# Optimization experiments

Measured on AMD Instinct MI355X. Metric: run time of the kernel, lower is better.

The kernel has to match this reference:

```python
import jax, jax.numpy as jnp
import numpy as np

P = 16384        # nodes per detector layer
NLAYERS = 5      # conf.nlayers (layer labels 0..NLAYERS)
NPROP = 1        # conf.model.nprop
D, S, H = 64, 16, 256   # dyn_features, static_features, deeplayer_nodes
E = 262144       # edges per edge-set (avg degree 16)
NG = 64          # num_graphs


def setup_inputs() -> dict:
    key = jax.random.key(0)
    ks = jax.random.split(key, 20)
    N = P * (NLAYERS + 1)
    F = D + S
    sc = 0.05
    ri = lambda k, shape: jax.random.randint(k, shape, 0, P, dtype=jnp.int32)
    return {
        "x0": jax.random.normal(ks[0], (N, 1), jnp.float32),
        "static": jax.random.normal(ks[1], (N, S), jnp.float32),
        "W1": jax.random.normal(ks[2], (4, F, H), jnp.float32) * sc,
        "b1": jax.random.normal(ks[3], (4, H), jnp.float32) * sc,
        "W2": jax.random.normal(ks[4], (4, H, H), jnp.float32) * sc,
        "b2": jax.random.normal(ks[5], (4, H), jnp.float32) * sc,
        "W3": jax.random.normal(ks[6], (4, H, D), jnp.float32) * sc,
        "b3": jax.random.normal(ks[7], (4, D), jnp.float32) * sc,
        "eps": jnp.zeros((3,), jnp.float32),
        "lin_w": jax.random.normal(ks[8], (D, 1), jnp.float32) * sc,
        "lin_b": jax.random.normal(ks[9], (1,), jnp.float32) * sc,
        "inner_src": ri(ks[10], (NLAYERS, E)),
        "inner_dst": ri(ks[11], (NLAYERS, E)),
        "fwd_src": ri(ks[12], (NLAYERS - 1, E)),
        "fwd_dst": ri(ks[13], (NLAYERS - 1, E)),
        "bwd_src": ri(ks[14], (NLAYERS - 1, E)),
        "bwd_dst": ri(ks[15], (NLAYERS - 1, E)),
        "batch_idx": jax.random.randint(ks[16], (N,), 0, NG, dtype=jnp.int32),
        "num_graphs": NG,
    }


def reference(x0, static, W1, b1, W2, b2, W3, b3, eps, lin_w, lin_b,
              inner_src, inner_dst, fwd_src, fwd_dst, bwd_src, bwd_dst,
              batch_idx, num_graphs):
    N = x0.shape[0]

    def mlp(i, h):
        # dnn(): Linear(F,H)+ReLU, Linear(H,H)+ReLU, Linear(H,D)+ReLU
        h = jax.nn.relu(h @ W1[i] + b1[i])
        h = jax.nn.relu(h @ W2[i] + b2[i])
        return jax.nn.relu(h @ W3[i] + b3[i])

    def gin(i, xs, src, dst):
        # GINConv(train_eps=True): mlp((1+eps)*x + sum_{j in N(v)} x_j)
        aggr = jax.ops.segment_sum(xs[src], dst, num_segments=xs.shape[0])
        return mlp(i, (1.0 + eps[i]) * xs + aggr)

    # x = hstack(batch.x, zeros(N, D-1))
    x = jnp.concatenate([x0, jnp.zeros((N, D - 1), x0.dtype)], axis=1)

    for _ in range(NPROP):
        for il in range(NLAYERS):
            s0 = il * P
            # inner conv on layer il (addstatic over that layer's nodes)
            xs = jnp.concatenate([x[s0:s0 + P], static[s0:s0 + P]], axis=1)
            x = x.at[s0:s0 + P].set(gin(0, xs, inner_src[il], inner_dst[il]))
            if il == NLAYERS - 1:
                continue
            # forward conv over layers il (local [0,P)) and il+1 (local [P,2P))
            xs2 = jnp.concatenate([x[s0:s0 + 2 * P], static[s0:s0 + 2 * P]], axis=1)
            out = gin(1, xs2, fwd_src[il], fwd_dst[il] + P)
            x = x.at[s0 + P:s0 + 2 * P].set(out[P:])
            # node_dnn on target layer
            xt = jnp.concatenate([x[s0 + P:s0 + 2 * P], static[s0 + P:s0 + 2 * P]], axis=1)
            x = x.at[s0 + P:s0 + 2 * P].set(mlp(3, xt))
        for il in range(NLAYERS - 1, 0, -1):
            s0 = (il - 1) * P
            # backward conv: layer il (local [P,2P)) -> layer il-1 (local [0,P))
            xs2 = jnp.concatenate([x[s0:s0 + 2 * P], static[s0:s0 + 2 * P]], axis=1)
            out = gin(2, xs2, bwd_src[il - 1] + P, bwd_dst[il - 1])
            x = x.at[s0:s0 + P].set(out[:P])
            # inner conv on layer il-1
            xs = jnp.concatenate([x[s0:s0 + P], static[s0:s0 + P]], axis=1)
            x = x.at[s0:s0 + P].set(gin(0, xs, inner_src[il - 1], inner_dst[il - 1]))
            # node_dnn on layer il-1
            xt = jnp.concatenate([x[s0:s0 + P], static[s0:s0 + P]], axis=1)
            x = x.at[s0:s0 + P].set(mlp(3, xt))

    pooled = jax.ops.segment_sum(x, batch_idx, num_segments=num_graphs)
    return jax.nn.relu(pooled @ lin_w + lin_b)
```

## Files before the change

### kernel.cpp

```cpp
#include <hip/hip_runtime.h>

#define P 16384
#define NLAYERS 5
#define NND 98304
#define D 64
#define S 16
#define F 80
#define KP1 96
#define H 256
#define EDG 262144
#define NG 64
#define NSETS 13
#define RSP 16385
#define LDP 40
#define LH2 264
#define LXS 100

typedef __attribute__((ext_vector_type(8))) _Float16 f16x8;
typedef __attribute__((ext_vector_type(4))) _Float16 f16x4;
typedef __attribute__((ext_vector_type(4))) float f32x4;

__device__ __forceinline__ void fatomic_add(float* p, float v) {
    unsafeAtomicAdd(p, v);
}

__global__ void k_init_x(const float* __restrict__ x0, float* __restrict__ X,
                         int* __restrict__ deg, float* __restrict__ PL) {
    int idx = blockIdx.x * blockDim.x + threadIdx.x;
    if (idx < NND * D) {
        int row = idx >> 6, f = idx & 63;
        X[idx] = (f == 0) ? x0[row] : 0.0f;
        return;
    }
    int r = idx - NND * D;
    if (r < NSETS * P) { deg[r] = 0; return; }
    r -= NSETS * P;
    if (r < NG * D) PL[r] = 0.0f;
}

__global__ void k_wconv_all(const float* __restrict__ W1, const float* __restrict__ W2,
                            const float* __restrict__ W3,
                            _Float16* __restrict__ w1, _Float16* __restrict__ w2,
                            _Float16* __restrict__ w3) {
    const int n1 = 4 * H * KP1, n2 = 4 * H * H, n3 = 4 * D * H;
    int idx = blockIdx.x * blockDim.x + threadIdx.x;
    const float* W; _Float16* h; int K, N, Kp, i;
    if (idx < n1)              { W = W1; h = w1; K = F; N = H; Kp = KP1; i = idx; }
    else if (idx < n1 + n2)    { W = W2; h = w2; K = H; N = H; Kp = H;   i = idx - n1; }
    else if (idx < n1 + n2 + n3){ W = W3; h = w3; K = H; N = D; Kp = H;  i = idx - n1 - n2; }
    else return;
    int set = i / (N * Kp), rem = i - set * (N * Kp);
    int n = rem / Kp, kp = rem - n * Kp;
    float v = (kp < K) ? W[(size_t)set * K * N + (size_t)kp * N + n] : 0.0f;
    h[i] = (_Float16)v;
}

__device__ __forceinline__ const int* set_ptr(int t, const int* inner, const int* fwd,
                                              const int* bwd) {
    if (t < 5) return inner + (size_t)t * EDG;
    if (t < 9) return fwd + (size_t)(t - 5) * EDG;
    return bwd + (size_t)(t - 9) * EDG;
}

__global__ void k_csr_hist(const int* __restrict__ inner_dst, const int* __restrict__ fwd_dst,
                           const int* __restrict__ bwd_dst, int* __restrict__ deg,
                           int* __restrict__ rank) {
    int idx = blockIdx.x * blockDim.x + threadIdx.x;
    if (idx >= NSETS * EDG) return;
    int t = idx >> 18, e = idx & (EDG - 1);
    const int* dstp = set_ptr(t, inner_dst, fwd_dst, bwd_dst);
    rank[idx] = atomicAdd(&deg[t * P + dstp[e]], 1);
}

__global__ __launch_bounds__(1024) void k_csr_scan(const int* __restrict__ deg,
                                                   int* __restrict__ rowstart) {
    __shared__ int part[1024];
    int t = blockIdx.x;
    const int* d = deg + t * P;
    int* rs = rowstart + (size_t)t * RSP;
    int tid = threadIdx.x;
    int base = tid * 16;
    int loc[16], sum = 0;
#pragma unroll
    for (int i = 0; i < 16; ++i) { loc[i] = sum; sum += d[base + i]; }
    part[tid] = sum;
    __syncthreads();
    for (int off = 1; off < 1024; off <<= 1) {
        int v = (tid >= off) ? part[tid - off] : 0;
        __syncthreads();
        part[tid] += v;
        __syncthreads();
    }
    int pre = tid ? part[tid - 1] : 0;
#pragma unroll
    for (int i = 0; i < 16; ++i) rs[base + i] = pre + loc[i];
    if (tid == 1023) rs[P] = pre + sum;
}

__global__ void k_csr_scatter(const int* __restrict__ inner_src, const int* __restrict__ inner_dst,
                              const int* __restrict__ fwd_src, const int* __restrict__ fwd_dst,
                              const int* __restrict__ bwd_src, const int* __restrict__ bwd_dst,
                              const int* __restrict__ rowstart, const int* __restrict__ rank,
                              int* __restrict__ elist) {
    int idx = blockIdx.x * blockDim.x + threadIdx.x;
    if (idx >= NSETS * EDG) return;
    int t = idx >> 18, e = idx & (EDG - 1);
    const int* srcp = set_ptr(t, inner_src, fwd_src, bwd_src);
    const int* dstp = set_ptr(t, inner_dst, fwd_dst, bwd_dst);
    int dv = dstp[e];
    elist[(size_t)t * EDG + rowstart[(size_t)t * RSP + dv] + rank[idx]] = srcp[e];
}

__global__ __launch_bounds__(256) void k_gather_T(const float* __restrict__ X,
                                                  const float* __restrict__ st,
                                                  const int* __restrict__ elist,
                                                  const int* __restrict__ rowstart,
                                                  _Float16* __restrict__ Th,
                                                  int dst_gbase, int src_gbase,
                                                  const float* __restrict__ eps, int ei) {
    int wv = threadIdx.x >> 6, l = threadIdx.x & 63;
    int v = blockIdx.x * 4 + wv;
    int beg = rowstart[v], end = rowstart[v + 1];
    float scale = 1.0f + eps[ei];
    int rg = l >> 4, c = l & 15;
    float ax0 = 0.f, ax1 = 0.f, ax2 = 0.f, ax3 = 0.f, as = 0.f;
    int i = beg;
    for (; i + 4 <= end; i += 4) {
        int s = src_gbase + elist[i + rg];
        float4 xv = *(const float4*)&X[(size_t)s * D + 4 * c];
        ax0 += xv.x; ax1 += xv.y; ax2 += xv.z; ax3 += xv.w;
        as += st[(size_t)s * S + c];
    }
    if (i < end) {
        int rem = end - i;
        if (rg < rem) {
            int s = src_gbase + elist[i + rg];
            float4 xv = *(const float4*)&X[(size_t)s * D + 4 * c];
            ax0 += xv.x; ax1 += xv.y; ax2 += xv.z; ax3 += xv.w;
            as += st[(size_t)s * S + c];
        }
    }
#pragma unroll
    for (int off = 16; off < 64; off <<= 1) {
        ax0 += __shfl_xor(ax0, off, 64);
        ax1 += __shfl_xor(ax1, off, 64);
        ax2 += __shfl_xor(ax2, off, 64);
        ax3 += __shfl_xor(ax3, off, 64);
        as  += __shfl_xor(as,  off, 64);
    }
    if (l < 16) {
        int g = dst_gbase + v;
        float4 sx = *(const float4*)&X[(size_t)g * D + 4 * l];
        f16x4 hv;
        hv[0] = (_Float16)(ax0 + scale * sx.x);
        hv[1] = (_Float16)(ax1 + scale * sx.y);
        hv[2] = (_Float16)(ax2 + scale * sx.z);
        hv[3] = (_Float16)(ax3 + scale * sx.w);
        *(f16x4*)&Th[(size_t)v * KP1 + 4 * l] = hv;
        Th[(size_t)v * KP1 + D + l] = (_Float16)(as + scale * st[(size_t)g * S + l]);
        Th[(size_t)v * KP1 + F + l] = (_Float16)0.0f;
    }
}

__global__ __launch_bounds__(512) void k_gemm1(
    const _Float16* __restrict__ Tp, int lda,
    const _Float16* __restrict__ Wp, int Kp,
    const float* __restrict__ bias,
    _Float16* __restrict__ Ch, int ldc)
{
    __shared__ _Float16 Ah[128][LDP];
    __shared__ _Float16 Bh[128][LDP];

    int tid = threadIdx.x;
    int lane = tid & 63, wid = tid >> 6;
    int wm = wid >> 2, wn = wid & 3;
    int m0 = blockIdx.y * 128, n0 = blockIdx.x * 128;

    f32x4 acc[4][2] = {};

    int ar = tid >> 2;
    int ac = (tid & 3) * 8;
    int la = lane & 15, lg = lane >> 4;

    for (int k0 = 0; k0 < Kp; k0 += 32) {
        *(f16x8*)&Ah[ar][ac] = *(const f16x8*)&Tp[(size_t)(m0 + ar) * lda + k0 + ac];
        *(f16x8*)&Bh[ar][ac] = *(const f16x8*)&Wp[(size_t)(n0 + ar) * Kp + k0 + ac];
        __syncthreads();

        int kf = lg * 8;
        f16x8 ah[4], bh[2];
#pragma unroll
        for (int m = 0; m < 4; ++m) ah[m] = *(const f16x8*)&Ah[wm * 64 + m * 16 + la][kf];
#pragma unroll
        for (int n = 0; n < 2; ++n) bh[n] = *(const f16x8*)&Bh[wn * 32 + n * 16 + la][kf];
#pragma unroll
        for (int m = 0; m < 4; ++m)
#pragma unroll
            for (int n = 0; n < 2; ++n)
                acc[m][n] = __builtin_amdgcn_mfma_f32_16x16x32_f16(ah[m], bh[n], acc[m][n], 0, 0, 0);
        __syncthreads();
    }

#pragma unroll
    for (int n = 0; n < 2; ++n) {
        int col = n0 + wn * 32 + n * 16 + la;
        float bv = bias[col];
#pragma unroll
        for (int m = 0; m < 4; ++m) {
            int row = m0 + wm * 64 + m * 16 + lg * 4;
#pragma unroll
            for (int r = 0; r < 4; ++r) {
                Ch[(size_t)(row + r) * ldc + col] = (_Float16)fmaxf(acc[m][n][r] + bv, 0.0f);
            }
        }
    }
}

template<int MODE>
__global__ __launch_bounds__(512, 4) void k_mlp23(
    const _Float16* __restrict__ H1p,
    const _Float16* __restrict__ W2p, const float* __restrict__ b2,
    const _Float16* __restrict__ W3p, const float* __restrict__ b3,
    float* __restrict__ Xout,
    const _Float16* __restrict__ W1p3, const float* __restrict__ b13,
    _Float16* __restrict__ H1o,
    int st_gbase, const float* __restrict__ stsrc)
{
    __shared__ _Float16 A1h[64][LDP];
    __shared__ _Float16 B1h[256][LDP];
    __shared__ _Float16 H2hs[64][LH2];
    __shared__ _Float16 Xsh[(MODE == 1) ? 64 : 1][LXS];

    int tid = threadIdx.x;
    int lane = tid & 63, wid = tid >> 6;
    int la = lane & 15, lg = lane >> 4;
    int r0 = blockIdx.x * 64;

    f32x4 acc[4][2] = {};
    for (int k0 = 0; k0 < H; k0 += 32) {
        if (tid < 256) {
            int ar = tid >> 2, aq = (tid & 3) * 8;
            *(f16x8*)&A1h[ar][aq] = *(const f16x8*)&H1p[(size_t)(r0 + ar) * H + k0 + aq];
        }
#pragma unroll
        for (int j = 0; j < 2; ++j) {
            int id = j * 512 + tid;
            int br = id >> 2, bq = (id & 3) * 8;
            *(f16x8*)&B1h[br][bq] = *(const f16x8*)&W2p[(size_t)br * H + k0 + bq];
        }
        __syncthreads();

        int kf = lg * 8;
        f16x8 ah[4], bh[2];
#pragma unroll
        for (int m = 0; m < 4; ++m) ah[m] = *(const f16x8*)&A1h[m * 16 + la][kf];
#pragma unroll
        for (int n = 0; n < 2; ++n) bh[n] = *(const f16x8*)&B1h[wid * 32 + n * 16 + la][kf];
#pragma unroll
        for (int m = 0; m < 4; ++m)
#pragma unroll
            for (int n = 0; n < 2; ++n)
                acc[m][n] = __builtin_amdgcn_mfma_f32_16x16x32_f16(ah[m], bh[n], acc[m][n], 0, 0, 0);
        __syncthreads();
    }
#pragma unroll
    for (int n = 0; n < 2; ++n) {
        int col = wid * 32 + n * 16 + la;
        float bv = b2[col];
#pragma unroll
        for (int m = 0; m < 4; ++m) {
            int row = m * 16 + lg * 4;
#pragma unroll
            for (int r = 0; r < 4; ++r) {
                H2hs[row + r][col] = (_Float16)fmaxf(acc[m][n][r] + bv, 0.0f);
            }
        }
    }
    __syncthreads();

    int wm = wid >> 2, wn = wid & 3;
    f32x4 acc2[2] = {};
    {
        for (int k0 = 0; k0 < H; k0 += 32) {
            if (tid < 256) {
                int br = tid >> 2, bq = (tid & 3) * 8;
                *(f16x8*)&B1h[br][bq] = *(const f16x8*)&W3p[(size_t)br * H + k0 + bq];
            }
            __syncthreads();

            int kf = lg * 8;
            f16x8 ah[2], bh;
#pragma unroll
            for (int m = 0; m < 2; ++m) ah[m] = *(const f16x8*)&H2hs[wm * 32 + m * 16 + la][k0 + kf];
            bh = *(const f16x8*)&B1h[wn * 16 + la][kf];
#pragma unroll
            for (int m = 0; m < 2; ++m)
                acc2[m] = __builtin_amdgcn_mfma_f32_16x16x32_f16(ah[m], bh, acc2[m], 0, 0, 0);
            __syncthreads();
        }
    }
    {
        int col = wn * 16 + la;
        float bv = b3[col];
#pragma unroll
        for (int m = 0; m < 2; ++m) {
            int rloc = wm * 32 + m * 16 + lg * 4;
#pragma unroll
            for (int r = 0; r < 4; ++r) {
                float v = fmaxf(acc2[m][r] + bv, 0.0f);
                if (MODE == 0) {
                    Xout[(size_t)(r0 + rloc + r) * D + col] = v;
                } else {
                    Xsh[rloc + r][col] = (_Float16)v;
                }
            }
        }
    }

    if (MODE == 1) {
        {
            int row = tid >> 3, c2 = (tid & 7) * 2;
            int g = st_gbase + r0 + row;
            float2 sv = *(const float2*)&stsrc[(size_t)g * S + c2];
            Xsh[row][D + c2] = (_Float16)sv.x;
            Xsh[row][D + c2 + 1] = (_Float16)sv.y;
            Xsh[row][F + c2] = (_Float16)0.0f;
            Xsh[row][F + c2 + 1] = (_Float16)0.0f;
        }
        __syncthreads();

        f32x4 acc4[4][2] = {};
        for (int k0 = 0; k0 < KP1; k0 += 32) {
#pragma unroll
            for (int j = 0; j < 2; ++j) {
                int id = j * 512 + tid;
                int br = id >> 2, bq = (id & 3) * 8;
                *(f16x8*)&B1h[br][bq] = *(const f16x8*)&W1p3[(size_t)br * KP1 + k0 + bq];
            }
            __syncthreads();

            int kf = lg * 8;
            f16x8 ah[4], bh[2];
#pragma unroll
            for (int m = 0; m < 4; ++m) ah[m] = *(const f16x8*)&Xsh[m * 16 + la][k0 + kf];
#pragma unroll
            for (int n = 0; n < 2; ++n) bh[n] = *(const f16x8*)&B1h[wid * 32 + n * 16 + la][kf];
#pragma unroll
            for (int m = 0; m < 4; ++m)
#pragma unroll
                for (int n = 0; n < 2; ++n)
                    acc4[m][n] = __builtin_amdgcn_mfma_f32_16x16x32_f16(ah[m], bh[n], acc4[m][n], 0, 0, 0);
            __syncthreads();
        }
#pragma unroll
        for (int n = 0; n < 2; ++n) {
            int col = wid * 32 + n * 16 + la;
            float bv = b13[col];
#pragma unroll
            for (int m = 0; m < 4; ++m) {
                int row = r0 + m * 16 + lg * 4;
#pragma unroll
                for (int r = 0; r < 4; ++r) {
                    H1o[(size_t)(row + r) * H + col] = (_Float16)fmaxf(acc4[m][n][r] + bv, 0.0f);
                }
            }
        }
    }
}

#define PROWS 1024
__global__ __launch_bounds__(256) void k_pool2(const float* __restrict__ X,
                                               const int* __restrict__ bidx,
                                               float* __restrict__ PL) {
    __shared__ float lds[NG * D];
    int tid = threadIdx.x;
    for (int i = tid; i < NG * D; i += 256) lds[i] = 0.0f;
    __syncthreads();
    int base = blockIdx.x * PROWS;
    int f = tid & 63, rg = tid >> 6;
    for (int r = base + rg; r < base + PROWS; r += 4) {
        int g = bidx[r];
        atomicAdd(&lds[g * D + f], X[(size_t)r * D + f]);
    }
    __syncthreads();
    for (int i = tid; i < NG * D; i += 256) {
        float v = lds[i];
        if (v != 0.0f) fatomic_add(&PL[i], v);
    }
}

__global__ void k_final(const float* __restrict__ pooled, const float* __restrict__ lin_w,
                        const float* __restrict__ lin_b, float* __restrict__ out) {
    int g = threadIdx.x;
    if (g >= NG) return;
    float acc = lin_b[0];
#pragma unroll
    for (int d2 = 0; d2 < D; ++d2) acc += pooled[g * D + d2] * lin_w[d2];
    out[g] = fmaxf(acc, 0.0f);
}

extern "C" void kernel_launch(void* const* d_in, const int* in_sizes, int n_in,
                              void* d_out, int out_size, void* d_ws, size_t ws_size,
                              hipStream_t stream) {
    const float* x0    = (const float*)d_in[0];
    const float* stat  = (const float*)d_in[1];
    const float* W1    = (const float*)d_in[2];
    const float* b1    = (const float*)d_in[3];
    const float* W2    = (const float*)d_in[4];
    const float* b2    = (const float*)d_in[5];
    const float* W3    = (const float*)d_in[6];
    const float* b3    = (const float*)d_in[7];
    const float* eps   = (const float*)d_in[8];
    const float* lin_w = (const float*)d_in[9];
    const float* lin_b = (const float*)d_in[10];
    const int* inner_src = (const int*)d_in[11];
    const int* inner_dst = (const int*)d_in[12];
    const int* fwd_src   = (const int*)d_in[13];
    const int* fwd_dst   = (const int*)d_in[14];
    const int* bwd_src   = (const int*)d_in[15];
    const int* bwd_dst   = (const int*)d_in[16];
    const int* bidx      = (const int*)d_in[17];

    float* X  = (float*)d_ws;
    float* PL = X + (size_t)NND * D;
    _Float16* Th  = (_Float16*)(PL + NG * D);
    _Float16* H1p = Th + (size_t)P * KP1;
    _Float16* w1p = H1p + (size_t)P * H;
    _Float16* w2p = w1p + (size_t)4 * H * KP1;
    _Float16* w3p = w2p + (size_t)4 * H * H;
    int* deg      = (int*)(w3p + (size_t)4 * D * H);
    int* rowstart = deg + (size_t)NSETS * P;
    int* rank     = rowstart + (size_t)NSETS * RSP;
    int* elist    = rank + (size_t)NSETS * EDG;

    {
        int tot = NND * D + NSETS * P + NG * D;
        k_init_x<<<(tot + 255) / 256, 256, 0, stream>>>(x0, X, deg, PL);
    }
    {
        int tot = 4 * H * KP1 + 4 * H * H + 4 * D * H;
        k_wconv_all<<<(tot + 255) / 256, 256, 0, stream>>>(W1, W2, W3, w1p, w2p, w3p);
    }
    k_csr_hist<<<(NSETS * EDG) / 256, 256, 0, stream>>>(inner_dst, fwd_dst, bwd_dst, deg, rank);
    k_csr_scan<<<NSETS, 1024, 0, stream>>>(deg, rowstart);
    k_csr_scatter<<<(NSETS * EDG) / 256, 256, 0, stream>>>(inner_src, inner_dst, fwd_src, fwd_dst,
                                                           bwd_src, bwd_dst, rowstart, rank, elist);

    _Float16* w13p = w1p + (size_t)3 * H * KP1;
    const float* b13 = b1 + 3 * H;

    auto mlp23_plain = [&](int set, int gbase_out) {
        k_mlp23<0><<<P / 64, 512, 0, stream>>>(
            H1p,
            w2p + (size_t)set * H * H, b2 + set * H,
            w3p + (size_t)set * D * H, b3 + set * D,
            X + (size_t)gbase_out * D,
            nullptr, nullptr, nullptr, 0, nullptr);
    };
    auto mlp23_fused = [&](int set, int gbase_node) {
        k_mlp23<1><<<P / 64, 512, 0, stream>>>(
            H1p,
            w2p + (size_t)set * H * H, b2 + set * H,
            w3p + (size_t)set * D * H, b3 + set * D,
            nullptr,
            w13p, b13, H1p, gbase_node, stat);
    };
    auto gemm1 = [&](int set) {
        k_gemm1<<<dim3(H / 128, P / 128), 512, 0, stream>>>(
            Th, KP1,
            w1p + (size_t)set * H * KP1, KP1,
            b1 + set * H, H1p, H);
    };
    auto gather = [&](int t, int dst_gbase, int src_gbase, int ei) {
        k_gather_T<<<P / 4, 256, 0, stream>>>(
            X, stat, elist + (size_t)t * EDG, rowstart + (size_t)t * RSP,
            Th, dst_gbase, src_gbase, eps, ei);
    };

    for (int il = 0; il < NLAYERS; ++il) {
        int s0 = il * P;
        gather(il, s0, s0, 0);
        gemm1(0);
        mlp23_plain(0, s0);
        if (il == NLAYERS - 1) continue;
        gather(5 + il, s0 + P, s0, 1);
        gemm1(1);
        mlp23_fused(1, s0 + P);
        mlp23_plain(3, s0 + P);
    }
    for (int il = NLAYERS - 1; il >= 1; --il) {
        int s0 = (il - 1) * P;
        gather(9 + (il - 1), s0, s0 + P, 2);
        gemm1(2);
        mlp23_plain(2, s0);
        gather(il - 1, s0, s0, 0);
        gemm1(0);
        mlp23_fused(0, s0);
        mlp23_plain(3, s0);
    }

    k_pool2<<<NND / PROWS, 256, 0, stream>>>(X, bidx, PL);
    k_final<<<1, 64, 0, stream>>>(PL, lin_w, lin_b, (float*)d_out);
}
```

Before: 986.4 us.

## Fuse first MLP layer GEMM into the per-row-block MLP kernel

```diff
diff --git a/kernel.cpp b/kernel.cpp
--- a/kernel.cpp
+++ b/kernel.cpp
@@ -162,63 +162,10 @@
     }
 }
 
-__global__ __launch_bounds__(512) void k_gemm1(
-    const _Float16* __restrict__ Tp, int lda,
-    const _Float16* __restrict__ Wp, int Kp,
-    const float* __restrict__ bias,
-    _Float16* __restrict__ Ch, int ldc)
-{
-    __shared__ _Float16 Ah[128][LDP];
-    __shared__ _Float16 Bh[128][LDP];
-
-    int tid = threadIdx.x;
-    int lane = tid & 63, wid = tid >> 6;
-    int wm = wid >> 2, wn = wid & 3;
-    int m0 = blockIdx.y * 128, n0 = blockIdx.x * 128;
-
-    f32x4 acc[4][2] = {};
-
-    int ar = tid >> 2;
-    int ac = (tid & 3) * 8;
-    int la = lane & 15, lg = lane >> 4;
-
-    for (int k0 = 0; k0 < Kp; k0 += 32) {
-        *(f16x8*)&Ah[ar][ac] = *(const f16x8*)&Tp[(size_t)(m0 + ar) * lda + k0 + ac];
-        *(f16x8*)&Bh[ar][ac] = *(const f16x8*)&Wp[(size_t)(n0 + ar) * Kp + k0 + ac];
-        __syncthreads();
-
-        int kf = lg * 8;
-        f16x8 ah[4], bh[2];
-#pragma unroll
-        for (int m = 0; m < 4; ++m) ah[m] = *(const f16x8*)&Ah[wm * 64 + m * 16 + la][kf];
-#pragma unroll
-        for (int n = 0; n < 2; ++n) bh[n] = *(const f16x8*)&Bh[wn * 32 + n * 16 + la][kf];
-#pragma unroll
-        for (int m = 0; m < 4; ++m)
-#pragma unroll
-            for (int n = 0; n < 2; ++n)
-                acc[m][n] = __builtin_amdgcn_mfma_f32_16x16x32_f16(ah[m], bh[n], acc[m][n], 0, 0, 0);
-        __syncthreads();
-    }
-
-#pragma unroll
-    for (int n = 0; n < 2; ++n) {
-        int col = n0 + wn * 32 + n * 16 + la;
-        float bv = bias[col];
-#pragma unroll
-        for (int m = 0; m < 4; ++m) {
-            int row = m0 + wm * 64 + m * 16 + lg * 4;
-#pragma unroll
-            for (int r = 0; r < 4; ++r) {
-                Ch[(size_t)(row + r) * ldc + col] = (_Float16)fmaxf(acc[m][n][r] + bv, 0.0f);
-            }
-        }
-    }
-}
-
 template<int MODE>
-__global__ __launch_bounds__(512, 4) void k_mlp23(
-    const _Float16* __restrict__ H1p,
+__global__ __launch_bounds__(512, 2) void k_mlp123(
+    const _Float16* __restrict__ Tp,
+    const _Float16* __restrict__ W1p, const float* __restrict__ b1,
     const _Float16* __restrict__ W2p, const float* __restrict__ b2,
     const _Float16* __restrict__ W3p, const float* __restrict__ b3,
     float* __restrict__ Xout,
@@ -228,6 +175,7 @@
 {
     __shared__ _Float16 A1h[64][LDP];
     __shared__ _Float16 B1h[256][LDP];
+    __shared__ _Float16 H1s[64][LH2];
     __shared__ _Float16 H2hs[64][LH2];
     __shared__ _Float16 Xsh[(MODE == 1) ? 64 : 1][LXS];
 
@@ -236,12 +184,52 @@
     int la = lane & 15, lg = lane >> 4;
     int r0 = blockIdx.x * 64;
 
+    {
+        f32x4 acc0[4][2] = {};
+        for (int k0 = 0; k0 < KP1; k0 += 32) {
+            if (tid < 256) {
+                int ar = tid >> 2, aq = (tid & 3) * 8;
+                *(f16x8*)&A1h[ar][aq] = *(const f16x8*)&Tp[(size_t)(r0 + ar) * KP1 + k0 + aq];
+            }
+#pragma unroll
+            for (int j = 0; j < 2; ++j) {
+                int id = j * 512 + tid;
+                int br = id >> 2, bq = (id & 3) * 8;
+                *(f16x8*)&B1h[br][bq] = *(const f16x8*)&W1p[(size_t)br * KP1 + k0 + bq];
+            }
+            __syncthreads();
+
+            int kf = lg * 8;
+            f16x8 ah[4], bh[2];
+#pragma unroll
+            for (int m = 0; m < 4; ++m) ah[m] = *(const f16x8*)&A1h[m * 16 + la][kf];
+#pragma unroll
+            for (int n = 0; n < 2; ++n) bh[n] = *(const f16x8*)&B1h[wid * 32 + n * 16 + la][kf];
+#pragma unroll
+            for (int m = 0; m < 4; ++m)
+#pragma unroll
+                for (int n = 0; n < 2; ++n)
+                    acc0[m][n] = __builtin_amdgcn_mfma_f32_16x16x32_f16(ah[m], bh[n], acc0[m][n], 0, 0, 0);
+            __syncthreads();
+        }
+#pragma unroll
+        for (int n = 0; n < 2; ++n) {
+            int col = wid * 32 + n * 16 + la;
+            float bv = b1[col];
+#pragma unroll
+            for (int m = 0; m < 4; ++m) {
+                int row = m * 16 + lg * 4;
+#pragma unroll
+                for (int r = 0; r < 4; ++r) {
+                    H1s[row + r][col] = (_Float16)fmaxf(acc0[m][n][r] + bv, 0.0f);
+                }
+            }
+        }
+        __syncthreads();
+    }
+
     f32x4 acc[4][2] = {};
     for (int k0 = 0; k0 < H; k0 += 32) {
-        if (tid < 256) {
-            int ar = tid >> 2, aq = (tid & 3) * 8;
-            *(f16x8*)&A1h[ar][aq] = *(const f16x8*)&H1p[(size_t)(r0 + ar) * H + k0 + aq];
-        }
 #pragma unroll
         for (int j = 0; j < 2; ++j) {
             int id = j * 512 + tid;
@@ -253,7 +241,7 @@
         int kf = lg * 8;
         f16x8 ah[4], bh[2];
 #pragma unroll
-        for (int m = 0; m < 4; ++m) ah[m] = *(const f16x8*)&A1h[m * 16 + la][kf];
+        for (int m = 0; m < 4; ++m) ah[m] = *(const f16x8*)&H1s[m * 16 + la][k0 + kf];
 #pragma unroll
         for (int n = 0; n < 2; ++n) bh[n] = *(const f16x8*)&B1h[wid * 32 + n * 16 + la][kf];
 #pragma unroll
@@ -363,6 +351,96 @@
                 for (int r = 0; r < 4; ++r) {
                     H1o[(size_t)(row + r) * H + col] = (_Float16)fmaxf(acc4[m][n][r] + bv, 0.0f);
                 }
+            }
+        }
+    }
+}
+
+__global__ __launch_bounds__(512, 4) void k_mlp23(
+    const _Float16* __restrict__ H1p,
+    const _Float16* __restrict__ W2p, const float* __restrict__ b2,
+    const _Float16* __restrict__ W3p, const float* __restrict__ b3,
+    float* __restrict__ Xout)
+{
+    __shared__ _Float16 A1h[64][LDP];
+    __shared__ _Float16 B1h[256][LDP];
+    __shared__ _Float16 H2hs[64][LH2];
+
+    int tid = threadIdx.x;
+    int lane = tid & 63, wid = tid >> 6;
+    int la = lane & 15, lg = lane >> 4;
+    int r0 = blockIdx.x * 64;
+
+    f32x4 acc[4][2] = {};
+    for (int k0 = 0; k0 < H; k0 += 32) {
+        if (tid < 256) {
+            int ar = tid >> 2, aq = (tid & 3) * 8;
+            *(f16x8*)&A1h[ar][aq] = *(const f16x8*)&H1p[(size_t)(r0 + ar) * H + k0 + aq];
+        }
+#pragma unroll
+        for (int j = 0; j < 2; ++j) {
+            int id = j * 512 + tid;
+            int br = id >> 2, bq = (id & 3) * 8;
+            *(f16x8*)&B1h[br][bq] = *(const f16x8*)&W2p[(size_t)br * H + k0 + bq];
+        }
+        __syncthreads();
+
+        int kf = lg * 8;
+        f16x8 ah[4], bh[2];
+#pragma unroll
+        for (int m = 0; m < 4; ++m) ah[m] = *(const f16x8*)&A1h[m * 16 + la][kf];
+#pragma unroll
+        for (int n = 0; n < 2; ++n) bh[n] = *(const f16x8*)&B1h[wid * 32 + n * 16 + la][kf];
+#pragma unroll
+        for (int m = 0; m < 4; ++m)
+#pragma unroll
+            for (int n = 0; n < 2; ++n)
+                acc[m][n] = __builtin_amdgcn_mfma_f32_16x16x32_f16(ah[m], bh[n], acc[m][n], 0, 0, 0);
+        __syncthreads();
+    }
+#pragma unroll
+    for (int n = 0; n < 2; ++n) {
+        int col = wid * 32 + n * 16 + la;
+        float bv = b2[col];
+#pragma unroll
+        for (int m = 0; m < 4; ++m) {
+            int row = m * 16 + lg * 4;
+#pragma unroll
+            for (int r = 0; r < 4; ++r) {
+                H2hs[row + r][col] = (_Float16)fmaxf(acc[m][n][r] + bv, 0.0f);
+            }
+        }
+    }
+    __syncthreads();
+
+    int wm = wid >> 2, wn = wid & 3;
+    f32x4 acc2[2] = {};
+    for (int k0 = 0; k0 < H; k0 += 32) {
+        if (tid < 256) {
+            int br = tid >> 2, bq = (tid & 3) * 8;
+            *(f16x8*)&B1h[br][bq] = *(const f16x8*)&W3p[(size_t)br * H + k0 + bq];
+        }
+        __syncthreads();
+
+        int kf = lg * 8;
+        f16x8 ah[2], bh;
+#pragma unroll
+        for (int m = 0; m < 2; ++m) ah[m] = *(const f16x8*)&H2hs[wm * 32 + m * 16 + la][k0 + kf];
+        bh = *(const f16x8*)&B1h[wn * 16 + la][kf];
+#pragma unroll
+        for (int m = 0; m < 2; ++m)
+            acc2[m] = __builtin_amdgcn_mfma_f32_16x16x32_f16(ah[m], bh, acc2[m], 0, 0, 0);
+        __syncthreads();
+    }
+    {
+        int col = wn * 16 + la;
+        float bv = b3[col];
+#pragma unroll
+        for (int m = 0; m < 2; ++m) {
+            int rloc = wm * 32 + m * 16 + lg * 4;
+#pragma unroll
+            for (int r = 0; r < 4; ++r) {
+                Xout[(size_t)(r0 + rloc + r) * D + col] = fmaxf(acc2[m][r] + bv, 0.0f);
             }
         }
     }
@@ -449,27 +527,30 @@
     _Float16* w13p = w1p + (size_t)3 * H * KP1;
     const float* b13 = b1 + 3 * H;
 
-    auto mlp23_plain = [&](int set, int gbase_out) {
-        k_mlp23<0><<<P / 64, 512, 0, stream>>>(
-            H1p,
+    auto conv_plain = [&](int set, int gbase_out) {
+        k_mlp123<0><<<P / 64, 512, 0, stream>>>(
+            Th,
+            w1p + (size_t)set * H * KP1, b1 + set * H,
             w2p + (size_t)set * H * H, b2 + set * H,
             w3p + (size_t)set * D * H, b3 + set * D,
             X + (size_t)gbase_out * D,
             nullptr, nullptr, nullptr, 0, nullptr);
     };
-    auto mlp23_fused = [&](int set, int gbase_node) {
-        k_mlp23<1><<<P / 64, 512, 0, stream>>>(
-            H1p,
+    auto conv_fused = [&](int set, int gbase_node) {
+        k_mlp123<1><<<P / 64, 512, 0, stream>>>(
+            Th,
+            w1p + (size_t)set * H * KP1, b1 + set * H,
             w2p + (size_t)set * H * H, b2 + set * H,
             w3p + (size_t)set * D * H, b3 + set * D,
             nullptr,
             w13p, b13, H1p, gbase_node, stat);
     };
-    auto gemm1 = [&](int set) {
-        k_gemm1<<<dim3(H / 128, P / 128), 512, 0, stream>>>(
-            Th, KP1,
-            w1p + (size_t)set * H * KP1, KP1,
-            b1 + set * H, H1p, H);
+    auto node_dnn = [&](int gbase_out) {
+        k_mlp23<<<P / 64, 512, 0, stream>>>(
+            H1p,
+            w2p + (size_t)3 * H * H, b2 + 3 * H,
+            w3p + (size_t)3 * D * H, b3 + 3 * D,
+            X + (size_t)gbase_out * D);
     };
     auto gather = [&](int t, int dst_gbase, int src_gbase, int ei) {
         k_gather_T<<<P / 4, 256, 0, stream>>>(
@@ -480,23 +561,19 @@
     for (int il = 0; il < NLAYERS; ++il) {
         int s0 = il * P;
         gather(il, s0, s0, 0);
-        gemm1(0);
-        mlp23_plain(0, s0);
+        conv_plain(0, s0);
         if (il == NLAYERS - 1) continue;
         gather(5 + il, s0 + P, s0, 1);
-        gemm1(1);
-        mlp23_fused(1, s0 + P);
-        mlp23_plain(3, s0 + P);
+        conv_fused(1, s0 + P);
+        node_dnn(s0 + P);
     }
     for (int il = NLAYERS - 1; il >= 1; --il) {
         int s0 = (il - 1) * P;
         gather(9 + (il - 1), s0, s0 + P, 2);
-        gemm1(2);
-        mlp23_plain(2, s0);
+        conv_plain(2, s0);
         gather(il - 1, s0, s0, 0);
-        gemm1(0);
-        mlp23_fused(0, s0);
-        mlp23_plain(3, s0);
+        conv_fused(0, s0);
+        node_dnn(s0);
     }
 
     k_pool2<<<NND / PROWS, 256, 0, stream>>>(X, bidx, PL);
```

Result: faster. 923.7 us (-6.4%).
